# Performance work log

Measured on AMD Instinct MI355X. Metric: run time of the kernel, lower is better.

## Reference

```python
import jax, jax.numpy as jnp
import numpy as np

N_USERS = 100000
N_ITEMS = 50000
N_NODES = N_USERS + N_ITEMS
EMBED_DIM = 64
N_LAYERS = 3
NNZ = 2400000
BATCH = 16384


def setup_inputs() -> dict:
    key = jax.random.key(0)
    ks = jax.random.split(key, 8)
    user_embed_weight = jax.random.normal(ks[0], (N_USERS, EMBED_DIM), dtype=jnp.float32) * 0.1
    item_embed_weight = jax.random.normal(ks[1], (N_ITEMS, EMBED_DIM), dtype=jnp.float32) * 0.1
    adj_row = jax.random.randint(ks[2], (NNZ,), 0, N_NODES, dtype=jnp.int32)
    adj_col = jax.random.randint(ks[3], (NNZ,), 0, N_NODES, dtype=jnp.int32)
    # positive normalized-ish edge weights (stand-in for D^-1/2 A D^-1/2 values)
    adj_vals = jax.random.uniform(ks[4], (NNZ,), dtype=jnp.float32) * 0.1
    users = jax.random.randint(ks[5], (BATCH,), 0, N_USERS, dtype=jnp.int32)
    pos_items = jax.random.randint(ks[6], (BATCH,), 0, N_ITEMS, dtype=jnp.int32)
    neg_items = jax.random.randint(ks[7], (BATCH,), 0, N_ITEMS, dtype=jnp.int32)
    return {
        "user_embed_weight": user_embed_weight,
        "item_embed_weight": item_embed_weight,
        "adj_vals": adj_vals,
        "adj_row": adj_row,
        "adj_col": adj_col,
        "users": users,
        "pos_items": pos_items,
        "neg_items": neg_items,
    }


def _spmm(vals, row, col, x, n):
    # sparse [n,n] @ dense [n,d] via gather + segment-sum
    return jax.ops.segment_sum(vals[:, None] * x[col], row, num_segments=n)


def reference(user_embed_weight, item_embed_weight, adj_vals, adj_row, adj_col,
              users, pos_items, neg_items):
    n = user_embed_weight.shape[0] + item_embed_weight.shape[0]
    all_embed = jnp.concatenate([user_embed_weight, item_embed_weight], axis=0)
    acc = all_embed
    x = all_embed
    for _ in range(N_LAYERS):
        x = _spmm(adj_vals, adj_row, adj_col, x, n)
        acc = acc + x
    final_embed = acc / (N_LAYERS + 1)
    user_emb = final_embed[: user_embed_weight.shape[0]]
    item_emb = final_embed[user_embed_weight.shape[0]:]

    u = user_emb[users]
    p = item_emb[pos_items]
    nn_ = item_emb[neg_items]
    pos_score = jnp.sum(u * p, axis=1)
    neg_score = jnp.sum(u * nn_, axis=1)
    loss = -jnp.mean(jnp.log(jax.nn.sigmoid(pos_score - neg_score) + 1e-08))
    reg_loss = (jnp.sum(user_embed_weight[users] ** 2)
                + jnp.sum(item_embed_weight[pos_items] ** 2)
                + jnp.sum(item_embed_weight[neg_items] ** 2)) / users.shape[0]
    return (loss, reg_loss)
```

## Files before the change

kernel.cpp:

```cpp
#include <hip/hip_runtime.h>

#define N_USERS 100000
#define N_ITEMS 50000
#define N_NODES (N_USERS + N_ITEMS)
#define DIM 64
#define BATCH 16384
#define RPB 512
#define BSHIFT 9
#define NB ((N_NODES + RPB - 1) / RPB)
#define HP 296
#define EPT 8
#define TILE_E (512 * EPT)
#define STRIDE 12288
#define XSCALE 64.0f
#define INV_XSCALE 0.015625f

struct __align__(8) Pair { int c; float v; };
typedef float floatx2 __attribute__((ext_vector_type(2)));

__device__ __forceinline__ unsigned pk8(float a, float b, float c, float d) {
    int w = __builtin_amdgcn_cvt_pk_fp8_f32(a, b, 0, false);
    w = __builtin_amdgcn_cvt_pk_fp8_f32(c, d, w, true);
    return (unsigned)w;
}

#define EDGE_F8D(V, X) { \
    floatx2 lo_ = __builtin_amdgcn_cvt_pk_f32_fp8((X), false); \
    floatx2 hi_ = __builtin_amdgcn_cvt_pk_f32_fp8((X), true); \
    a0 = fmaf((V), lo_.x, a0); a1 = fmaf((V), lo_.y, a1); \
    a2 = fmaf((V), hi_.x, a2); a3 = fmaf((V), hi_.y, a3); }

__device__ __forceinline__ Pair ldnt(const Pair* p) {
    unsigned long long w = __builtin_nontemporal_load((const unsigned long long*)p);
    Pair r;
    r.c = (int)(unsigned)(w & 0xffffffffu);
    r.v = __uint_as_float((unsigned)(w >> 32));
    return r;
}

__device__ __forceinline__ float block_reduce_sum(float v) {
    for (int s = 32; s > 0; s >>= 1) v += __shfl_xor(v, s, 64);
    __shared__ float sm[8];
    int lane = threadIdx.x & 63;
    int wid  = threadIdx.x >> 6;
    if (lane == 0) sm[wid] = v;
    __syncthreads();
    float t = 0.0f;
    if (threadIdx.x == 0) {
        int nw = (blockDim.x + 63) >> 6;
        for (int w = 0; w < nw; ++w) t += sm[w];
    }
    return t;
}

__global__ void convert_kernel(const float* __restrict__ uw, const float* __restrict__ iw,
                               unsigned char* __restrict__ x8,
                               int* __restrict__ flags, int* __restrict__ bcursor,
                               float* __restrict__ sums) {
    size_t tid = (size_t)blockIdx.x * 256 + threadIdx.x;
    if (tid < 2) sums[tid] = 0.0f;
    if (tid < N_NODES) flags[tid] = 0;
    else if (tid < N_NODES + NB) bcursor[tid - N_NODES] = 0;
    size_t base = tid * 8;
    if (base >= (size_t)N_NODES * DIM) return;
    const float* src = (base < (size_t)N_USERS * DIM) ? uw + base
                                                      : iw + (base - (size_t)N_USERS * DIM);
    float4 a = ((const float4*)src)[0];
    float4 b = ((const float4*)src)[1];
    uint2 o;
    o.x = pk8(XSCALE * a.x, XSCALE * a.y, XSCALE * a.z, XSCALE * a.w);
    o.y = pk8(XSCALE * b.x, XSCALE * b.y, XSCALE * b.z, XSCALE * b.w);
    *(uint2*)(x8 + base) = o;
}

__global__ void init_kernel(const float* __restrict__ uw, const float* __restrict__ iw,
                            const int* __restrict__ users, const int* __restrict__ pos,
                            const int* __restrict__ neg,
                            float* __restrict__ uacc, float* __restrict__ pacc,
                            float* __restrict__ nacc, float* __restrict__ reg_sum,
                            int* __restrict__ flags) {
    int tid = blockIdx.x * blockDim.x + threadIdx.x;
    if (tid < BATCH)          flags[users[tid]] = 1;
    else if (tid < 2 * BATCH) flags[N_USERS + pos[tid - BATCH]] = 1;
    else if (tid < 3 * BATCH) flags[N_USERS + neg[tid - 2 * BATCH]] = 1;
    int i = tid >> 4;
    int q = tid & 15;
    if (i >= BATCH) return;
    size_t o = (size_t)i * DIM + q * 4;
    float4 u = *(const float4*)(uw + (size_t)users[i] * DIM + q * 4);
    float4 p = *(const float4*)(iw + (size_t)pos[i]   * DIM + q * 4);
    float4 n = *(const float4*)(iw + (size_t)neg[i]   * DIM + q * 4);
    *(float4*)(uacc + o) = u;
    *(float4*)(pacc + o) = p;
    *(float4*)(nacc + o) = n;
    float ss = u.x*u.x + u.y*u.y + u.z*u.z + u.w*u.w
             + p.x*p.x + p.y*p.y + p.z*p.z + p.w*p.w
             + n.x*n.x + n.y*n.y + n.z*n.z + n.w*n.w;
    float bt = block_reduce_sum(ss);
    if (threadIdx.x == 0) unsafeAtomicAdd(reg_sum, bt);
}

__global__ void binned_scatter_kernel(const int* __restrict__ rows, const int* __restrict__ cols,
                                      const float* __restrict__ vals, int* __restrict__ bcursor,
                                      Pair* __restrict__ bcv, int nnz) {
    __shared__ int h[8][HP];
    int t = threadIdx.x, w = t >> 6;
    for (int i = t; i < 8 * HP; i += 512) ((int*)h)[i] = 0;
    __syncthreads();
    long long tile = (long long)blockIdx.x * TILE_E;
    int er[EPT], cr[EPT];
    float vr[EPT];
    #pragma unroll
    for (int j = 0; j < EPT; ++j) {
        long long e = tile + t + j * 512;
        if (e < nnz) {
            int r = rows[e];
            er[j] = r;
            cr[j] = cols[e];
            vr[j] = vals[e];
            atomicAdd(&h[w][r >> BSHIFT], 1);
        } else er[j] = -1;
    }
    __syncthreads();
    for (int b = t; b < NB; b += 512) {
        int cw[8], tot = 0;
        #pragma unroll
        for (int w2 = 0; w2 < 8; ++w2) { cw[w2] = h[w2][b]; tot += cw[w2]; }
        int base = tot ? (b * STRIDE + atomicAdd(&bcursor[b], tot)) : 0;
        #pragma unroll
        for (int w2 = 0; w2 < 8; ++w2) { h[w2][b] = base; base += cw[w2]; }
    }
    __syncthreads();
    #pragma unroll
    for (int j = 0; j < EPT; ++j) {
        if (er[j] >= 0) {
            int r = er[j];
            int dst = atomicAdd(&h[w][r >> BSHIFT], 1);
            Pair p;
            p.c = cr[j] | ((r & (RPB - 1)) << 18);
            p.v = vr[j];
            bcv[dst] = p;
        }
    }
}

__global__ void post_scan_kernel(const int* __restrict__ counts, int* __restrict__ bbase,
                                 int* __restrict__ rowptr, int nnz) {
    __shared__ int sm[512];
    int t = threadIdx.x;
    int v = (t < NB) ? counts[t] : 0;
    sm[t] = v;
    __syncthreads();
    for (int off = 1; off < 512; off <<= 1) {
        int tmp = (t >= off) ? sm[t - off] : 0;
        __syncthreads();
        sm[t] += tmp;
        __syncthreads();
    }
    if (t < NB) bbase[t] = sm[t] - v;
    if (t == 511) bbase[NB] = sm[511];
    if (t == 0) rowptr[N_NODES] = nnz;
}

__global__ void bucket_sort_kernel(const Pair* __restrict__ bcv,
                                   const int* __restrict__ counts,
                                   const int* __restrict__ bbase,
                                   int* __restrict__ rowptr, Pair* __restrict__ perm) {
    __shared__ int rh8[8][RPB + 8];
    __shared__ int rh[RPB];
    __shared__ int sc[RPB];
    int blk = blockIdx.x;
    int t = threadIdx.x;
    int w = t >> 6;
    size_t src = (size_t)blk * STRIDE;
    int base = bbase[blk];
    int cnt  = counts[blk];
    for (int i = t; i < 8 * (RPB + 8); i += 512) ((int*)rh8)[i] = 0;
    __syncthreads();
    for (int i = t; i < cnt; i += 512)
        atomicAdd(&rh8[w][(unsigned)bcv[src + i].c >> 18], 1);
    __syncthreads();
    int v = 0;
    #pragma unroll
    for (int w2 = 0; w2 < 8; ++w2) v += rh8[w2][t];
    sc[t] = v;
    __syncthreads();
    for (int off = 1; off < 512; off <<= 1) {
        int tmp = (t >= off) ? sc[t - off] : 0;
        __syncthreads();
        sc[t] += tmp;
        __syncthreads();
    }
    int excl = sc[t] - v;
    int g = blk * RPB + t;
    if (g < N_NODES) rowptr[g] = base + excl;
    rh[t] = excl;
    __syncthreads();
    for (int i = t; i < cnt; i += 512) {
        Pair p = bcv[src + i];
        int r = (unsigned)p.c >> 18;
        int rk = atomicAdd(&rh[r], 1);
        p.c &= 0x3FFFF;
        perm[base + rk] = p;
    }
}

template<bool FLAGGED>
__global__ void spmm_csr_f8_kernel(const unsigned char* __restrict__ x8,
                                   const Pair* __restrict__ pe,
                                   const int* __restrict__ rowptr,
                                   const int* __restrict__ flags,
                                   unsigned char* __restrict__ out8) {
    int row = blockIdx.x * 16 + (threadIdx.x >> 4);
    if (row >= N_NODES) return;
    if (FLAGGED && !flags[row]) return;
    int q = threadIdx.x & 15;
    int start = rowptr[row];
    int end   = rowptr[row + 1];
    float a0 = 0.f, a1 = 0.f, a2 = 0.f, a3 = 0.f;
    int e = start;
    for (; e + 7 < end; e += 8) {
        Pair p0 = ldnt(pe + e),     p1 = ldnt(pe + e + 1);
        Pair p2 = ldnt(pe + e + 2), p3 = ldnt(pe + e + 3);
        Pair p4 = ldnt(pe + e + 4), p5 = ldnt(pe + e + 5);
        Pair p6 = ldnt(pe + e + 6), p7 = ldnt(pe + e + 7);
        unsigned x0 = *(const unsigned*)(x8 + ((size_t)p0.c << 6) + q * 4);
        unsigned x1 = *(const unsigned*)(x8 + ((size_t)p1.c << 6) + q * 4);
        unsigned x2 = *(const unsigned*)(x8 + ((size_t)p2.c << 6) + q * 4);
        unsigned x3 = *(const unsigned*)(x8 + ((size_t)p3.c << 6) + q * 4);
        unsigned x4 = *(const unsigned*)(x8 + ((size_t)p4.c << 6) + q * 4);
        unsigned x5 = *(const unsigned*)(x8 + ((size_t)p5.c << 6) + q * 4);
        unsigned x6 = *(const unsigned*)(x8 + ((size_t)p6.c << 6) + q * 4);
        unsigned x7 = *(const unsigned*)(x8 + ((size_t)p7.c << 6) + q * 4);
        EDGE_F8D(p0.v, x0); EDGE_F8D(p1.v, x1);
        EDGE_F8D(p2.v, x2); EDGE_F8D(p3.v, x3);
        EDGE_F8D(p4.v, x4); EDGE_F8D(p5.v, x5);
        EDGE_F8D(p6.v, x6); EDGE_F8D(p7.v, x7);
    }
    for (; e + 1 < end; e += 2) {
        Pair p0 = ldnt(pe + e), p1 = ldnt(pe + e + 1);
        unsigned x0 = *(const unsigned*)(x8 + ((size_t)p0.c << 6) + q * 4);
        unsigned x1 = *(const unsigned*)(x8 + ((size_t)p1.c << 6) + q * 4);
        EDGE_F8D(p0.v, x0); EDGE_F8D(p1.v, x1);
    }
    if (e < end) {
        Pair p = ldnt(pe + e);
        unsigned x = *(const unsigned*)(x8 + ((size_t)p.c << 6) + q * 4);
        EDGE_F8D(p.v, x);
    }
    *(unsigned*)(out8 + ((size_t)row << 6) + q * 4) = pk8(a0, a1, a2, a3);
}

__global__ void spmm_atomic_kernel(const float* __restrict__ xu, const float* __restrict__ xi,
                                   const float* __restrict__ vals, const int* __restrict__ rows,
                                   const int* __restrict__ cols,
                                   float* __restrict__ out, int nnz) {
    long long tid = (long long)blockIdx.x * blockDim.x + threadIdx.x;
    int e = (int)(tid >> 4);
    if (e >= nnz) return;
    int q = (int)(tid & 15);
    int r = rows[e];
    int c = cols[e];
    float v = vals[e];
    const float* src = (c < N_USERS) ? (xu + (size_t)c * DIM)
                                     : (xi + (size_t)(c - N_USERS) * DIM);
    float4 x = *(const float4*)(src + q * 4);
    float* dst = out + (size_t)r * DIM + q * 4;
    unsafeAtomicAdd(dst + 0, v * x.x);
    unsafeAtomicAdd(dst + 1, v * x.y);
    unsafeAtomicAdd(dst + 2, v * x.z);
    unsafeAtomicAdd(dst + 3, v * x.w);
}

__global__ void gather_add_f8_kernel(const unsigned char* __restrict__ x8,
                                     const int* __restrict__ users, const int* __restrict__ pos,
                                     const int* __restrict__ neg,
                                     float* __restrict__ uacc, float* __restrict__ pacc,
                                     float* __restrict__ nacc) {
    int tid = blockIdx.x * blockDim.x + threadIdx.x;
    int i = tid >> 4;
    int q = tid & 15;
    if (i >= BATCH) return;
    size_t o = (size_t)i * DIM + q * 4;
    float4 a;
    unsigned u;
    floatx2 lo, hi;

    a = *(float4*)(uacc + o);
    u = *(const unsigned*)(x8 + ((size_t)users[i] << 6) + q * 4);
    lo = __builtin_amdgcn_cvt_pk_f32_fp8(u, false);
    hi = __builtin_amdgcn_cvt_pk_f32_fp8(u, true);
    a.x = fmaf(lo.x, INV_XSCALE, a.x); a.y = fmaf(lo.y, INV_XSCALE, a.y);
    a.z = fmaf(hi.x, INV_XSCALE, a.z); a.w = fmaf(hi.y, INV_XSCALE, a.w);
    *(float4*)(uacc + o) = a;

    a = *(float4*)(pacc + o);
    u = *(const unsigned*)(x8 + ((size_t)(N_USERS + pos[i]) << 6) + q * 4);
    lo = __builtin_amdgcn_cvt_pk_f32_fp8(u, false);
    hi = __builtin_amdgcn_cvt_pk_f32_fp8(u, true);
    a.x = fmaf(lo.x, INV_XSCALE, a.x); a.y = fmaf(lo.y, INV_XSCALE, a.y);
    a.z = fmaf(hi.x, INV_XSCALE, a.z); a.w = fmaf(hi.y, INV_XSCALE, a.w);
    *(float4*)(pacc + o) = a;

    a = *(float4*)(nacc + o);
    u = *(const unsigned*)(x8 + ((size_t)(N_USERS + neg[i]) << 6) + q * 4);
    lo = __builtin_amdgcn_cvt_pk_f32_fp8(u, false);
    hi = __builtin_amdgcn_cvt_pk_f32_fp8(u, true);
    a.x = fmaf(lo.x, INV_XSCALE, a.x); a.y = fmaf(lo.y, INV_XSCALE, a.y);
    a.z = fmaf(hi.x, INV_XSCALE, a.z); a.w = fmaf(hi.y, INV_XSCALE, a.w);
    *(float4*)(nacc + o) = a;
}

__global__ void gather_score_kernel(const unsigned char* __restrict__ x8,
                                    const int* __restrict__ users, const int* __restrict__ pos,
                                    const int* __restrict__ neg,
                                    const float* __restrict__ uacc, const float* __restrict__ pacc,
                                    const float* __restrict__ nacc, float* __restrict__ loss_sum) {
    int tid = blockIdx.x * blockDim.x + threadIdx.x;
    int i = tid >> 4;
    int q = tid & 15;
    float ps = 0.0f, ns = 0.0f;
    if (i < BATCH) {
        size_t o = (size_t)i * DIM + q * 4;
        float4 u = *(const float4*)(uacc + o);
        float4 p = *(const float4*)(pacc + o);
        float4 n = *(const float4*)(nacc + o);
        unsigned t;
        floatx2 lo, hi;
        t = *(const unsigned*)(x8 + ((size_t)users[i] << 6) + q * 4);
        lo = __builtin_amdgcn_cvt_pk_f32_fp8(t, false);
        hi = __builtin_amdgcn_cvt_pk_f32_fp8(t, true);
        u.x = fmaf(lo.x, INV_XSCALE, u.x); u.y = fmaf(lo.y, INV_XSCALE, u.y);
        u.z = fmaf(hi.x, INV_XSCALE, u.z); u.w = fmaf(hi.y, INV_XSCALE, u.w);
        t = *(const unsigned*)(x8 + ((size_t)(N_USERS + pos[i]) << 6) + q * 4);
        lo = __builtin_amdgcn_cvt_pk_f32_fp8(t, false);
        hi = __builtin_amdgcn_cvt_pk_f32_fp8(t, true);
        p.x = fmaf(lo.x, INV_XSCALE, p.x); p.y = fmaf(lo.y, INV_XSCALE, p.y);
        p.z = fmaf(hi.x, INV_XSCALE, p.z); p.w = fmaf(hi.y, INV_XSCALE, p.w);
        t = *(const unsigned*)(x8 + ((size_t)(N_USERS + neg[i]) << 6) + q * 4);
        lo = __builtin_amdgcn_cvt_pk_f32_fp8(t, false);
        hi = __builtin_amdgcn_cvt_pk_f32_fp8(t, true);
        n.x = fmaf(lo.x, INV_XSCALE, n.x); n.y = fmaf(lo.y, INV_XSCALE, n.y);
        n.z = fmaf(hi.x, INV_XSCALE, n.z); n.w = fmaf(hi.y, INV_XSCALE, n.w);
        ps = u.x*p.x + u.y*p.y + u.z*p.z + u.w*p.w;
        ns = u.x*n.x + u.y*n.y + u.z*n.z + u.w*n.w;
    }
    for (int s = 8; s > 0; s >>= 1) {
        ps += __shfl_xor(ps, s, 16);
        ns += __shfl_xor(ns, s, 16);
    }
    float term = 0.0f;
    if (q == 0 && i < BATCH) {
        float d = (ps - ns) * (1.0f / 16.0f);
        float sig = 1.0f / (1.0f + expf(-d));
        term = logf(sig + 1e-8f);
    }
    float bt = block_reduce_sum(term);
    if (threadIdx.x == 0) unsafeAtomicAdd(loss_sum, bt);
}

__global__ void gather_add_kernel(const float* __restrict__ x,
                                  const int* __restrict__ users, const int* __restrict__ pos,
                                  const int* __restrict__ neg,
                                  float* __restrict__ uacc, float* __restrict__ pacc,
                                  float* __restrict__ nacc) {
    int tid = blockIdx.x * blockDim.x + threadIdx.x;
    int i = tid >> 4;
    int q = tid & 15;
    if (i >= BATCH) return;
    size_t o = (size_t)i * DIM + q * 4;
    float4 a, b;
    a = *(float4*)(uacc + o);
    b = *(const float4*)(x + (size_t)users[i] * DIM + q * 4);
    a.x += b.x; a.y += b.y; a.z += b.z; a.w += b.w;
    *(float4*)(uacc + o) = a;
    a = *(float4*)(pacc + o);
    b = *(const float4*)(x + (size_t)(N_USERS + pos[i]) * DIM + q * 4);
    a.x += b.x; a.y += b.y; a.z += b.z; a.w += b.w;
    *(float4*)(pacc + o) = a;
    a = *(float4*)(nacc + o);
    b = *(const float4*)(x + (size_t)(N_USERS + neg[i]) * DIM + q * 4);
    a.x += b.x; a.y += b.y; a.z += b.z; a.w += b.w;
    *(float4*)(nacc + o) = a;
}

__global__ void score_kernel(const float* __restrict__ uacc, const float* __restrict__ pacc,
                             const float* __restrict__ nacc, float* __restrict__ loss_sum) {
    int tid = blockIdx.x * blockDim.x + threadIdx.x;
    int i = tid >> 4;
    int q = tid & 15;
    float ps = 0.0f, ns = 0.0f;
    if (i < BATCH) {
        size_t o = (size_t)i * DIM + q * 4;
        float4 u = *(const float4*)(uacc + o);
        float4 p = *(const float4*)(pacc + o);
        float4 n = *(const float4*)(nacc + o);
        ps = u.x*p.x + u.y*p.y + u.z*p.z + u.w*p.w;
        ns = u.x*n.x + u.y*n.y + u.z*n.z + u.w*n.w;
    }
    for (int s = 8; s > 0; s >>= 1) {
        ps += __shfl_xor(ps, s, 16);
        ns += __shfl_xor(ns, s, 16);
    }
    float term = 0.0f;
    if (q == 0 && i < BATCH) {
        float d = (ps - ns) * (1.0f / 16.0f);
        float sig = 1.0f / (1.0f + expf(-d));
        term = logf(sig + 1e-8f);
    }
    float bt = block_reduce_sum(term);
    if (threadIdx.x == 0) unsafeAtomicAdd(loss_sum, bt);
}

__global__ void finalize_kernel(const float* __restrict__ sums, float* __restrict__ out) {
    if (threadIdx.x == 0 && blockIdx.x == 0) {
        out[0] = -sums[0] / (float)BATCH;
        out[1] =  sums[1] / (float)BATCH;
    }
}

static inline size_t align256(size_t x) { return (x + 255) & ~(size_t)255; }

extern "C" void kernel_launch(void* const* d_in, const int* in_sizes, int n_in,
                              void* d_out, int out_size, void* d_ws, size_t ws_size,
                              hipStream_t stream) {
    const float* uw   = (const float*)d_in[0];
    const float* iw   = (const float*)d_in[1];
    const float* vals = (const float*)d_in[2];
    const int*   rows = (const int*)d_in[3];
    const int*   cols = (const int*)d_in[4];
    const int*   users = (const int*)d_in[5];
    const int*   pos   = (const int*)d_in[6];
    const int*   neg   = (const int*)d_in[7];
    const int nnz = in_sizes[2];

    char* ws = (char*)d_ws;
    const size_t nodeBytes = (size_t)N_NODES * DIM * sizeof(float);
    const size_t qBytes    = (size_t)N_NODES * DIM;
    const size_t accBytes  = (size_t)BATCH * DIM * sizeof(float);

    size_t off = 0;
    char*  nodeReg = ws + off;            off += align256(2 * nodeBytes);
    float* uacc = (float*)(ws + off);     off += align256(accBytes);
    float* pacc = (float*)(ws + off);     off += align256(accBytes);
    float* nacc = (float*)(ws + off);     off += align256(accBytes);
    float* sums = (float*)(ws + off);     off += 256;
    Pair*  perm = (Pair*)(ws + off);      off += align256((size_t)nnz * sizeof(Pair));
    int*   rowptr = (int*)(ws + off);     off += align256((size_t)(N_NODES + 1) * sizeof(int));
    int*   bbase  = (int*)(ws + off);     off += align256((size_t)(NB + 1) * sizeof(int));
    int*   bcursor= (int*)(ws + off);     off += align256((size_t)NB * sizeof(int));
    int*   flags  = (int*)(ws + off);     off += align256((size_t)N_NODES * sizeof(int));
    const bool fits_alias = (2 * align256(qBytes) + (size_t)NB * STRIDE * sizeof(Pair)) <= 2 * nodeBytes;
    const bool use_csr = (off <= ws_size) && fits_alias && (N_NODES < (1 << 18));

    unsigned char* xb0 = (unsigned char*)nodeReg;
    unsigned char* xb1 = (unsigned char*)(nodeReg + align256(qBytes));
    unsigned char* xb2 = (unsigned char*)(nodeReg + 2 * align256(qBytes));
    Pair*          bcv = (Pair*)(nodeReg + 2 * align256(qBytes));
    float* xA = (float*)nodeReg;
    float* xB = (float*)(nodeReg + nodeBytes);

    float* out = (float*)d_out;

    const int bthreads = BATCH * 16;
    const int bblocks  = bthreads / 256;
    const int tblocks  = (nnz + TILE_E - 1) / TILE_E;
    const int cblocks  = (int)(((size_t)N_NODES * DIM / 8 + 255) / 256);

    if (use_csr) {
        convert_kernel<<<cblocks, 256, 0, stream>>>(uw, iw, xb0, flags, bcursor, sums);
        init_kernel<<<bblocks, 256, 0, stream>>>(uw, iw, users, pos, neg, uacc, pacc, nacc, sums + 1, flags);
        binned_scatter_kernel<<<tblocks, 512, 0, stream>>>(rows, cols, vals, bcursor, bcv, nnz);
        post_scan_kernel<<<1, 512, 0, stream>>>(bcursor, bbase, rowptr, nnz);
        bucket_sort_kernel<<<NB, 512, 0, stream>>>(bcv, bcursor, bbase, rowptr, perm);

        const int sblocks = (N_NODES + 15) / 16;
        spmm_csr_f8_kernel<false><<<sblocks, 256, 0, stream>>>(xb0, perm, rowptr, flags, xb1);
        gather_add_f8_kernel<<<bblocks, 256, 0, stream>>>(xb1, users, pos, neg, uacc, pacc, nacc);
        spmm_csr_f8_kernel<false><<<sblocks, 256, 0, stream>>>(xb1, perm, rowptr, flags, xb2);
        gather_add_f8_kernel<<<bblocks, 256, 0, stream>>>(xb2, users, pos, neg, uacc, pacc, nacc);
        spmm_csr_f8_kernel<true><<<sblocks, 256, 0, stream>>>(xb2, perm, rowptr, flags, xb0);
        gather_score_kernel<<<bblocks, 256, 0, stream>>>(xb0, users, pos, neg, uacc, pacc, nacc, sums);
    } else {
        const long long sthreads = (long long)nnz * 16;
        const int sblocks = (int)((sthreads + 255) / 256);
        (void)hipMemsetAsync(sums, 0, 2 * sizeof(float), stream);
        init_kernel<<<bblocks, 256, 0, stream>>>(uw, iw, users, pos, neg, uacc, pacc, nacc, sums + 1, flags);
        (void)hipMemsetAsync(xA, 0, nodeBytes, stream);
        spmm_atomic_kernel<<<sblocks, 256, 0, stream>>>(uw, iw, vals, rows, cols, xA, nnz);
        gather_add_kernel<<<bblocks, 256, 0, stream>>>(xA, users, pos, neg, uacc, pacc, nacc);
        (void)hipMemsetAsync(xB, 0, nodeBytes, stream);
        spmm_atomic_kernel<<<sblocks, 256, 0, stream>>>(xA, xA + (size_t)N_USERS * DIM, vals, rows, cols, xB, nnz);
        gather_add_kernel<<<bblocks, 256, 0, stream>>>(xB, users, pos, neg, uacc, pacc, nacc);
        (void)hipMemsetAsync(xA, 0, nodeBytes, stream);
        spmm_atomic_kernel<<<sblocks, 256, 0, stream>>>(xB, xB + (size_t)N_USERS * DIM, vals, rows, cols, xA, nnz);
        gather_add_kernel<<<bblocks, 256, 0, stream>>>(xA, users, pos, neg, uacc, pacc, nacc);
        score_kernel<<<bblocks, 256, 0, stream>>>(uacc, pacc, nacc, sums);
    }

    finalize_kernel<<<1, 1, 0, stream>>>(sums, out);
}
```

Baseline: 250.5 us.

## Fuse gather-add into SpMM launches, compact final layer worklist, fold finalize into score

Merges each gather_add pass into the following SpMM launch as extra blocks, so the gather over the previous layer's output overlaps with the next layer's SpMM and launch count drops. The last layer now runs only over a compacted worklist of batch-referenced rows, built with atomicExch/atomicAdd in init, instead of launching a full grid that early-exits on flags. The finalize kernel is removed by having the last score block compute the output via a ticket counter. The SpMM inner loop is also software-pipelined, prefetching the next 8 edge pairs while gathering the current ones. In exchange, worklist construction adds atomics and the pipelined loop uses more registers.

```diff
diff --git a/kernel.cpp b/kernel.cpp
--- a/kernel.cpp
+++ b/kernel.cpp
@@ -14,6 +14,8 @@
 #define STRIDE 12288
 #define XSCALE 64.0f
 #define INV_XSCALE 0.015625f
+#define SB ((N_NODES + 15) / 16)
+#define WLB ((3 * BATCH) / 16)
 
 struct __align__(8) Pair { int c; float v; };
 typedef float floatx2 __attribute__((ext_vector_type(2)));
@@ -29,6 +31,8 @@
     floatx2 hi_ = __builtin_amdgcn_cvt_pk_f32_fp8((X), true); \
     a0 = fmaf((V), lo_.x, a0); a1 = fmaf((V), lo_.y, a1); \
     a2 = fmaf((V), hi_.x, a2); a3 = fmaf((V), hi_.y, a3); }
+
+#define LDX(P) (*(const unsigned*)(x8 + ((size_t)(P).c << 6) + q * 4))
 
 __device__ __forceinline__ Pair ldnt(const Pair* p) {
     unsigned long long w = __builtin_nontemporal_load((const unsigned long long*)p);
@@ -56,9 +60,9 @@
 __global__ void convert_kernel(const float* __restrict__ uw, const float* __restrict__ iw,
                                unsigned char* __restrict__ x8,
                                int* __restrict__ flags, int* __restrict__ bcursor,
-                               float* __restrict__ sums) {
+                               float* __restrict__ sums, int* __restrict__ ctrl) {
     size_t tid = (size_t)blockIdx.x * 256 + threadIdx.x;
-    if (tid < 2) sums[tid] = 0.0f;
+    if (tid == 0) { sums[0] = 0.0f; sums[1] = 0.0f; ctrl[0] = 0; ctrl[1] = 0; }
     if (tid < N_NODES) flags[tid] = 0;
     else if (tid < N_NODES + NB) bcursor[tid - N_NODES] = 0;
     size_t base = tid * 8;
@@ -73,16 +77,21 @@
     *(uint2*)(x8 + base) = o;
 }
 
+template<bool DOWL>
 __global__ void init_kernel(const float* __restrict__ uw, const float* __restrict__ iw,
                             const int* __restrict__ users, const int* __restrict__ pos,
                             const int* __restrict__ neg,
                             float* __restrict__ uacc, float* __restrict__ pacc,
                             float* __restrict__ nacc, float* __restrict__ reg_sum,
-                            int* __restrict__ flags) {
+                            int* __restrict__ flags, int* __restrict__ wl,
+                            int* __restrict__ ctrl) {
     int tid = blockIdx.x * blockDim.x + threadIdx.x;
-    if (tid < BATCH)          flags[users[tid]] = 1;
-    else if (tid < 2 * BATCH) flags[N_USERS + pos[tid - BATCH]] = 1;
-    else if (tid < 3 * BATCH) flags[N_USERS + neg[tid - 2 * BATCH]] = 1;
+    if (DOWL && tid < 3 * BATCH) {
+        int r = (tid < BATCH) ? users[tid]
+              : (tid < 2 * BATCH) ? N_USERS + pos[tid - BATCH]
+              : N_USERS + neg[tid - 2 * BATCH];
+        if (atomicExch(&flags[r], 1) == 0) wl[atomicAdd(&ctrl[0], 1)] = r;
+    }
     int i = tid >> 4;
     int q = tid & 15;
     if (i >= BATCH) return;
@@ -205,50 +214,128 @@
     }
 }
 
-template<bool FLAGGED>
-__global__ void spmm_csr_f8_kernel(const unsigned char* __restrict__ x8,
-                                   const Pair* __restrict__ pe,
-                                   const int* __restrict__ rowptr,
-                                   const int* __restrict__ flags,
-                                   unsigned char* __restrict__ out8) {
+__device__ __forceinline__ void spmm_row_f8(const unsigned char* __restrict__ x8,
+                                            const Pair* __restrict__ pe,
+                                            int e, int end, int q, int row,
+                                            unsigned char* __restrict__ out8) {
+    float a0 = 0.f, a1 = 0.f, a2 = 0.f, a3 = 0.f;
+    if (e + 8 <= end) {
+        Pair c0 = ldnt(pe+e),   c1 = ldnt(pe+e+1), c2 = ldnt(pe+e+2), c3 = ldnt(pe+e+3),
+             c4 = ldnt(pe+e+4), c5 = ldnt(pe+e+5), c6 = ldnt(pe+e+6), c7 = ldnt(pe+e+7);
+        e += 8;
+        for (; e + 8 <= end; e += 8) {
+            unsigned x0 = LDX(c0), x1 = LDX(c1), x2 = LDX(c2), x3 = LDX(c3),
+                     x4 = LDX(c4), x5 = LDX(c5), x6 = LDX(c6), x7 = LDX(c7);
+            Pair n0 = ldnt(pe+e),   n1 = ldnt(pe+e+1), n2 = ldnt(pe+e+2), n3 = ldnt(pe+e+3),
+                 n4 = ldnt(pe+e+4), n5 = ldnt(pe+e+5), n6 = ldnt(pe+e+6), n7 = ldnt(pe+e+7);
+            EDGE_F8D(c0.v, x0); EDGE_F8D(c1.v, x1);
+            EDGE_F8D(c2.v, x2); EDGE_F8D(c3.v, x3);
+            EDGE_F8D(c4.v, x4); EDGE_F8D(c5.v, x5);
+            EDGE_F8D(c6.v, x6); EDGE_F8D(c7.v, x7);
+            c0 = n0; c1 = n1; c2 = n2; c3 = n3;
+            c4 = n4; c5 = n5; c6 = n6; c7 = n7;
+        }
+        unsigned x0 = LDX(c0), x1 = LDX(c1), x2 = LDX(c2), x3 = LDX(c3),
+                 x4 = LDX(c4), x5 = LDX(c5), x6 = LDX(c6), x7 = LDX(c7);
+        EDGE_F8D(c0.v, x0); EDGE_F8D(c1.v, x1);
+        EDGE_F8D(c2.v, x2); EDGE_F8D(c3.v, x3);
+        EDGE_F8D(c4.v, x4); EDGE_F8D(c5.v, x5);
+        EDGE_F8D(c6.v, x6); EDGE_F8D(c7.v, x7);
+    }
+    for (; e < end; ++e) {
+        Pair p = ldnt(pe + e);
+        unsigned x = LDX(p);
+        EDGE_F8D(p.v, x);
+    }
+    *(unsigned*)(out8 + ((size_t)row << 6) + q * 4) = pk8(a0, a1, a2, a3);
+}
+
+__device__ __forceinline__ void gather_add_body(int tid, const unsigned char* __restrict__ x8,
+                                                const int* __restrict__ users,
+                                                const int* __restrict__ pos,
+                                                const int* __restrict__ neg,
+                                                float* __restrict__ uacc,
+                                                float* __restrict__ pacc,
+                                                float* __restrict__ nacc) {
+    int i = tid >> 4;
+    int q = tid & 15;
+    if (i >= BATCH) return;
+    size_t o = (size_t)i * DIM + q * 4;
+    float4 a;
+    unsigned u;
+    floatx2 lo, hi;
+
+    a = *(float4*)(uacc + o);
+    u = *(const unsigned*)(x8 + ((size_t)users[i] << 6) + q * 4);
+    lo = __builtin_amdgcn_cvt_pk_f32_fp8(u, false);
+    hi = __builtin_amdgcn_cvt_pk_f32_fp8(u, true);
+    a.x = fmaf(lo.x, INV_XSCALE, a.x); a.y = fmaf(lo.y, INV_XSCALE, a.y);
+    a.z = fmaf(hi.x, INV_XSCALE, a.z); a.w = fmaf(hi.y, INV_XSCALE, a.w);
+    *(float4*)(uacc + o) = a;
+
+    a = *(float4*)(pacc + o);
+    u = *(const unsigned*)(x8 + ((size_t)(N_USERS + pos[i]) << 6) + q * 4);
+    lo = __builtin_amdgcn_cvt_pk_f32_fp8(u, false);
+    hi = __builtin_amdgcn_cvt_pk_f32_fp8(u, true);
+    a.x = fmaf(lo.x, INV_XSCALE, a.x); a.y = fmaf(lo.y, INV_XSCALE, a.y);
+    a.z = fmaf(hi.x, INV_XSCALE, a.z); a.w = fmaf(hi.y, INV_XSCALE, a.w);
+    *(float4*)(pacc + o) = a;
+
+    a = *(float4*)(nacc + o);
+    u = *(const unsigned*)(x8 + ((size_t)(N_USERS + neg[i]) << 6) + q * 4);
+    lo = __builtin_amdgcn_cvt_pk_f32_fp8(u, false);
+    hi = __builtin_amdgcn_cvt_pk_f32_fp8(u, true);
+    a.x = fmaf(lo.x, INV_XSCALE, a.x); a.y = fmaf(lo.y, INV_XSCALE, a.y);
+    a.z = fmaf(hi.x, INV_XSCALE, a.z); a.w = fmaf(hi.y, INV_XSCALE, a.w);
+    *(float4*)(nacc + o) = a;
+}
+
+__global__ void spmm_f8_kernel(const unsigned char* __restrict__ x8,
+                               const Pair* __restrict__ pe,
+                               const int* __restrict__ rowptr,
+                               unsigned char* __restrict__ out8) {
     int row = blockIdx.x * 16 + (threadIdx.x >> 4);
     if (row >= N_NODES) return;
-    if (FLAGGED && !flags[row]) return;
-    int q = threadIdx.x & 15;
-    int start = rowptr[row];
-    int end   = rowptr[row + 1];
-    float a0 = 0.f, a1 = 0.f, a2 = 0.f, a3 = 0.f;
-    int e = start;
-    for (; e + 7 < end; e += 8) {
-        Pair p0 = ldnt(pe + e),     p1 = ldnt(pe + e + 1);
-        Pair p2 = ldnt(pe + e + 2), p3 = ldnt(pe + e + 3);
-        Pair p4 = ldnt(pe + e + 4), p5 = ldnt(pe + e + 5);
-        Pair p6 = ldnt(pe + e + 6), p7 = ldnt(pe + e + 7);
-        unsigned x0 = *(const unsigned*)(x8 + ((size_t)p0.c << 6) + q * 4);
-        unsigned x1 = *(const unsigned*)(x8 + ((size_t)p1.c << 6) + q * 4);
-        unsigned x2 = *(const unsigned*)(x8 + ((size_t)p2.c << 6) + q * 4);
-        unsigned x3 = *(const unsigned*)(x8 + ((size_t)p3.c << 6) + q * 4);
-        unsigned x4 = *(const unsigned*)(x8 + ((size_t)p4.c << 6) + q * 4);
-        unsigned x5 = *(const unsigned*)(x8 + ((size_t)p5.c << 6) + q * 4);
-        unsigned x6 = *(const unsigned*)(x8 + ((size_t)p6.c << 6) + q * 4);
-        unsigned x7 = *(const unsigned*)(x8 + ((size_t)p7.c << 6) + q * 4);
-        EDGE_F8D(p0.v, x0); EDGE_F8D(p1.v, x1);
-        EDGE_F8D(p2.v, x2); EDGE_F8D(p3.v, x3);
-        EDGE_F8D(p4.v, x4); EDGE_F8D(p5.v, x5);
-        EDGE_F8D(p6.v, x6); EDGE_F8D(p7.v, x7);
-    }
-    for (; e + 1 < end; e += 2) {
-        Pair p0 = ldnt(pe + e), p1 = ldnt(pe + e + 1);
-        unsigned x0 = *(const unsigned*)(x8 + ((size_t)p0.c << 6) + q * 4);
-        unsigned x1 = *(const unsigned*)(x8 + ((size_t)p1.c << 6) + q * 4);
-        EDGE_F8D(p0.v, x0); EDGE_F8D(p1.v, x1);
-    }
-    if (e < end) {
-        Pair p = ldnt(pe + e);
-        unsigned x = *(const unsigned*)(x8 + ((size_t)p.c << 6) + q * 4);
-        EDGE_F8D(p.v, x);
-    }
-    *(unsigned*)(out8 + ((size_t)row << 6) + q * 4) = pk8(a0, a1, a2, a3);
+    spmm_row_f8(x8, pe, rowptr[row], rowptr[row + 1], threadIdx.x & 15, row, out8);
+}
+
+__global__ void spmm_gather_f8_kernel(const unsigned char* __restrict__ xsrc,
+                                      const Pair* __restrict__ pe,
+                                      const int* __restrict__ rowptr,
+                                      unsigned char* __restrict__ out8,
+                                      const int* __restrict__ users, const int* __restrict__ pos,
+                                      const int* __restrict__ neg,
+                                      float* __restrict__ uacc, float* __restrict__ pacc,
+                                      float* __restrict__ nacc) {
+    if (blockIdx.x < SB) {
+        int row = blockIdx.x * 16 + (threadIdx.x >> 4);
+        if (row >= N_NODES) return;
+        spmm_row_f8(xsrc, pe, rowptr[row], rowptr[row + 1], threadIdx.x & 15, row, out8);
+    } else {
+        gather_add_body((blockIdx.x - SB) * 256 + threadIdx.x, xsrc,
+                        users, pos, neg, uacc, pacc, nacc);
+    }
+}
+
+__global__ void spmm_wl_gather_f8_kernel(const unsigned char* __restrict__ xsrc,
+                                         const Pair* __restrict__ pe,
+                                         const int* __restrict__ rowptr,
+                                         unsigned char* __restrict__ out8,
+                                         const int* __restrict__ wl,
+                                         const int* __restrict__ ctrl,
+                                         const int* __restrict__ users, const int* __restrict__ pos,
+                                         const int* __restrict__ neg,
+                                         float* __restrict__ uacc, float* __restrict__ pacc,
+                                         float* __restrict__ nacc) {
+    if (blockIdx.x < WLB) {
+        int idx = blockIdx.x * 16 + (threadIdx.x >> 4);
+        if (idx >= ctrl[0]) return;
+        int row = wl[idx];
+        spmm_row_f8(xsrc, pe, rowptr[row], rowptr[row + 1], threadIdx.x & 15, row, out8);
+    } else {
+        gather_add_body((blockIdx.x - WLB) * 256 + threadIdx.x, xsrc,
+                        users, pos, neg, uacc, pacc, nacc);
+    }
 }
 
 __global__ void spmm_atomic_kernel(const float* __restrict__ xu, const float* __restrict__ xi,
@@ -272,50 +359,12 @@
     unsafeAtomicAdd(dst + 3, v * x.w);
 }
 
-__global__ void gather_add_f8_kernel(const unsigned char* __restrict__ x8,
-                                     const int* __restrict__ users, const int* __restrict__ pos,
-                                     const int* __restrict__ neg,
-                                     float* __restrict__ uacc, float* __restrict__ pacc,
-                                     float* __restrict__ nacc) {
-    int tid = blockIdx.x * blockDim.x + threadIdx.x;
-    int i = tid >> 4;
-    int q = tid & 15;
-    if (i >= BATCH) return;
-    size_t o = (size_t)i * DIM + q * 4;
-    float4 a;
-    unsigned u;
-    floatx2 lo, hi;
-
-    a = *(float4*)(uacc + o);
-    u = *(const unsigned*)(x8 + ((size_t)users[i] << 6) + q * 4);
-    lo = __builtin_amdgcn_cvt_pk_f32_fp8(u, false);
-    hi = __builtin_amdgcn_cvt_pk_f32_fp8(u, true);
-    a.x = fmaf(lo.x, INV_XSCALE, a.x); a.y = fmaf(lo.y, INV_XSCALE, a.y);
-    a.z = fmaf(hi.x, INV_XSCALE, a.z); a.w = fmaf(hi.y, INV_XSCALE, a.w);
-    *(float4*)(uacc + o) = a;
-
-    a = *(float4*)(pacc + o);
-    u = *(const unsigned*)(x8 + ((size_t)(N_USERS + pos[i]) << 6) + q * 4);
-    lo = __builtin_amdgcn_cvt_pk_f32_fp8(u, false);
-    hi = __builtin_amdgcn_cvt_pk_f32_fp8(u, true);
-    a.x = fmaf(lo.x, INV_XSCALE, a.x); a.y = fmaf(lo.y, INV_XSCALE, a.y);
-    a.z = fmaf(hi.x, INV_XSCALE, a.z); a.w = fmaf(hi.y, INV_XSCALE, a.w);
-    *(float4*)(pacc + o) = a;
-
-    a = *(float4*)(nacc + o);
-    u = *(const unsigned*)(x8 + ((size_t)(N_USERS + neg[i]) << 6) + q * 4);
-    lo = __builtin_amdgcn_cvt_pk_f32_fp8(u, false);
-    hi = __builtin_amdgcn_cvt_pk_f32_fp8(u, true);
-    a.x = fmaf(lo.x, INV_XSCALE, a.x); a.y = fmaf(lo.y, INV_XSCALE, a.y);
-    a.z = fmaf(hi.x, INV_XSCALE, a.z); a.w = fmaf(hi.y, INV_XSCALE, a.w);
-    *(float4*)(nacc + o) = a;
-}
-
 __global__ void gather_score_kernel(const unsigned char* __restrict__ x8,
                                     const int* __restrict__ users, const int* __restrict__ pos,
                                     const int* __restrict__ neg,
                                     const float* __restrict__ uacc, const float* __restrict__ pacc,
-                                    const float* __restrict__ nacc, float* __restrict__ loss_sum) {
+                                    const float* __restrict__ nacc, float* __restrict__ sums,
+                                    int* __restrict__ ctrl, float* __restrict__ out) {
     int tid = blockIdx.x * blockDim.x + threadIdx.x;
     int i = tid >> 4;
     int q = tid & 15;
@@ -356,7 +405,17 @@
         term = logf(sig + 1e-8f);
     }
     float bt = block_reduce_sum(term);
-    if (threadIdx.x == 0) unsafeAtomicAdd(loss_sum, bt);
+    if (threadIdx.x == 0) {
+        unsafeAtomicAdd(&sums[0], bt);
+        __threadfence();
+        int tk = atomicAdd(&ctrl[1], 1);
+        if (tk == (int)gridDim.x - 1) {
+            float ls = unsafeAtomicAdd(&sums[0], 0.0f);
+            float rs = unsafeAtomicAdd(&sums[1], 0.0f);
+            out[0] = -ls / (float)BATCH;
+            out[1] =  rs / (float)BATCH;
+        }
+    }
 }
 
 __global__ void gather_add_kernel(const float* __restrict__ x,
@@ -445,11 +504,13 @@
     float* pacc = (float*)(ws + off);     off += align256(accBytes);
     float* nacc = (float*)(ws + off);     off += align256(accBytes);
     float* sums = (float*)(ws + off);     off += 256;
+    int*   ctrl = (int*)(ws + off);       off += 256;
     Pair*  perm = (Pair*)(ws + off);      off += align256((size_t)nnz * sizeof(Pair));
     int*   rowptr = (int*)(ws + off);     off += align256((size_t)(N_NODES + 1) * sizeof(int));
     int*   bbase  = (int*)(ws + off);     off += align256((size_t)(NB + 1) * sizeof(int));
     int*   bcursor= (int*)(ws + off);     off += align256((size_t)NB * sizeof(int));
     int*   flags  = (int*)(ws + off);     off += align256((size_t)N_NODES * sizeof(int));
+    int*   wl     = (int*)(ws + off);     off += align256((size_t)(3 * BATCH) * sizeof(int));
     const bool fits_alias = (2 * align256(qBytes) + (size_t)NB * STRIDE * sizeof(Pair)) <= 2 * nodeBytes;
     const bool use_csr = (off <= ws_size) && fits_alias && (N_NODES < (1 << 18));
 
@@ -468,24 +529,28 @@
     const int cblocks  = (int)(((size_t)N_NODES * DIM / 8 + 255) / 256);
 
     if (use_csr) {
-        convert_kernel<<<cblocks, 256, 0, stream>>>(uw, iw, xb0, flags, bcursor, sums);
-        init_kernel<<<bblocks, 256, 0, stream>>>(uw, iw, users, pos, neg, uacc, pacc, nacc, sums + 1, flags);
+        convert_kernel<<<cblocks, 256, 0, stream>>>(uw, iw, xb0, flags, bcursor, sums, ctrl);
+        init_kernel<true><<<bblocks, 256, 0, stream>>>(uw, iw, users, pos, neg,
+                                                       uacc, pacc, nacc, sums + 1, flags, wl, ctrl);
         binned_scatter_kernel<<<tblocks, 512, 0, stream>>>(rows, cols, vals, bcursor, bcv, nnz);
         post_scan_kernel<<<1, 512, 0, stream>>>(bcursor, bbase, rowptr, nnz);
         bucket_sort_kernel<<<NB, 512, 0, stream>>>(bcv, bcursor, bbase, rowptr, perm);
 
-        const int sblocks = (N_NODES + 15) / 16;
-        spmm_csr_f8_kernel<false><<<sblocks, 256, 0, stream>>>(xb0, perm, rowptr, flags, xb1);
-        gather_add_f8_kernel<<<bblocks, 256, 0, stream>>>(xb1, users, pos, neg, uacc, pacc, nacc);
-        spmm_csr_f8_kernel<false><<<sblocks, 256, 0, stream>>>(xb1, perm, rowptr, flags, xb2);
-        gather_add_f8_kernel<<<bblocks, 256, 0, stream>>>(xb2, users, pos, neg, uacc, pacc, nacc);
-        spmm_csr_f8_kernel<true><<<sblocks, 256, 0, stream>>>(xb2, perm, rowptr, flags, xb0);
-        gather_score_kernel<<<bblocks, 256, 0, stream>>>(xb0, users, pos, neg, uacc, pacc, nacc, sums);
+        spmm_f8_kernel<<<SB, 256, 0, stream>>>(xb0, perm, rowptr, xb1);
+        spmm_gather_f8_kernel<<<SB + bblocks, 256, 0, stream>>>(xb1, perm, rowptr, xb2,
+                                                                users, pos, neg, uacc, pacc, nacc);
+        spmm_wl_gather_f8_kernel<<<WLB + bblocks, 256, 0, stream>>>(xb2, perm, rowptr, xb0,
+                                                                    wl, ctrl, users, pos, neg,
+                                                                    uacc, pacc, nacc);
+        gather_score_kernel<<<bblocks, 256, 0, stream>>>(xb0, users, pos, neg,
+                                                         uacc, pacc, nacc, sums, ctrl, out);
     } else {
         const long long sthreads = (long long)nnz * 16;
         const int sblocks = (int)((sthreads + 255) / 256);
         (void)hipMemsetAsync(sums, 0, 2 * sizeof(float), stream);
-        init_kernel<<<bblocks, 256, 0, stream>>>(uw, iw, users, pos, neg, uacc, pacc, nacc, sums + 1, flags);
+        (void)hipMemsetAsync(ctrl, 0, 2 * sizeof(int), stream);
+        init_kernel<false><<<bblocks, 256, 0, stream>>>(uw, iw, users, pos, neg,
+                                                        uacc, pacc, nacc, sums + 1, flags, wl, ctrl);
         (void)hipMemsetAsync(xA, 0, nodeBytes, stream);
         spmm_atomic_kernel<<<sblocks, 256, 0, stream>>>(uw, iw, vals, rows, cols, xA, nnz);
         gather_add_kernel<<<bblocks, 256, 0, stream>>>(xA, users, pos, neg, uacc, pacc, nacc);
@@ -496,7 +561,6 @@
         spmm_atomic_kernel<<<sblocks, 256, 0, stream>>>(xB, xB + (size_t)N_USERS * DIM, vals, rows, cols, xA, nnz);
         gather_add_kernel<<<bblocks, 256, 0, stream>>>(xA, users, pos, neg, uacc, pacc, nacc);
         score_kernel<<<bblocks, 256, 0, stream>>>(uacc, pacc, nacc, sums);
-    }
-
-    finalize_kernel<<<1, 1, 0, stream>>>(sums, out);
-}
+        finalize_kernel<<<1, 1, 0, stream>>>(sums, out);
+    }
+}
```

Result: slower. 271.7 us (+8.5%).
